# Kernel tuning notes

Measured on AMD Instinct MI355X. Metric: run time of the kernel, lower is better.

The kernel has to match this reference:

```python
import jax, jax.numpy as jnp
import numpy as np

N, E, IN, OUT = 50000, 800000, 128, 128
R = 5  # num_rels + 1 (last slice is the self-loop weight)


def setup_inputs() -> dict:
    key = jax.random.key(0)
    k = jax.random.split(key, 6)
    x = jax.random.normal(k[0], (N, IN), jnp.float32)
    src = jax.random.randint(k[1], (E,), 0, N)
    dst = jax.random.randint(k[2], (E,), 0, N)
    rel = jax.random.randint(k[3], (E,), 0, R - 1)  # edge rel_type in [0, num_rels)
    xavier = np.sqrt(2.0) * np.sqrt(6.0 / (IN + OUT))  # gain('relu') * xavier bound scale
    weight = jax.random.uniform(k[4], (R, IN, OUT), jnp.float32, -xavier, xavier)
    bias = jax.random.uniform(k[5], (R, OUT), jnp.float32, -xavier, xavier)
    return dict(x=x, weight=weight, bias=bias, src=src, dst=dst, rel=rel)


def reference(x, weight, bias, src, dst, rel):
    num_nodes = x.shape[0]
    num_edge_rels = weight.shape[0] - 1
    x_src = x[src]  # [E, IN] per-edge source gather
    # Per-edge message: x_src @ weight[rel] + bias[rel].
    # Grouped-GEMM style: one dense GEMM per relation, select by mask
    # (avoids materializing [E, IN, OUT] per-edge weights).
    msg = jnp.zeros((src.shape[0], weight.shape[2]), x.dtype)
    for r in range(num_edge_rels):
        hr = x_src @ weight[r] + bias[r]  # [E, OUT]
        msg = jnp.where((rel == r)[:, None], hr, msg)
    # Max-aggregation onto destination nodes; DGL fills 0 for nodes w/o in-edges.
    agg = jax.ops.segment_max(msg, dst, num_segments=num_nodes)  # [N, OUT]
    deg = jax.ops.segment_sum(jnp.ones_like(dst, jnp.float32), dst, num_segments=num_nodes)
    agg = jnp.where((deg > 0)[:, None], agg, jnp.zeros((), x.dtype))
    # Self-loop transform with last weight/bias slice.
    h = x @ weight[-1] + bias[-1] + agg
    return h
```

## Files before the change

### kernel.cpp

```cpp
#include <hip/hip_runtime.h>

#define NNODES 50000
#define NEDGES 800000
#define DIM    128
#define NRELS  4
#define NBLK2  25
#define DBLK   128
#define NDB    (5*DBLK)
#define NFB    3125
#define EPB    12500
#define NHC    64
#define RNG    25000
#define NPB    782

typedef __attribute__((ext_vector_type(8))) short bf16x8;
typedef __attribute__((ext_vector_type(8))) unsigned short u16x8;
typedef __attribute__((ext_vector_type(4))) float f32x4;

#define SSRC_OFF 0
#define CNT_OFF  3200000
#define BSUM_OFF 3404800
#define RANK_OFF 3405056
#define PCNT_OFF 5005056
#define WT_OFF   11405056
#define XBF_OFF  11568896
#define H_OFF    24368896

__device__ __forceinline__ unsigned short f2bf(float f) {
  unsigned u = __float_as_uint(f);
  return (unsigned short)((u + 0x7FFFu + ((u >> 16) & 1u)) >> 16);
}

__global__ __launch_bounds__(1024) void k_ph(
    const float* __restrict__ x, unsigned short* __restrict__ xbf,
    const float* __restrict__ W, unsigned short* __restrict__ Wt,
    const int* __restrict__ dst, unsigned short* __restrict__ rank,
    unsigned short* __restrict__ pcnt) {
  __shared__ unsigned lh[RNG / 2];
  if (blockIdx.x < NHC * 2) {
    int c = blockIdx.x >> 1;
    int r0 = (blockIdx.x & 1) * RNG;
    for (int i = threadIdx.x; i < RNG / 2; i += 1024) lh[i] = 0u;
    __syncthreads();
    int e0 = c * EPB;
    for (int e = e0 + threadIdx.x; e < e0 + EPB; e += 1024) {
      int d = dst[e] - r0;
      if ((unsigned)d < (unsigned)RNG) {
        unsigned old = atomicAdd(&lh[d >> 1], (d & 1) ? 65536u : 1u);
        rank[e] = (unsigned short)((old >> ((d & 1) << 4)) & 0xFFFFu);
      }
    }
    __syncthreads();
    unsigned* prow = (unsigned*)(pcnt + (size_t)c * NNODES + r0);
    for (int i = threadIdx.x; i < RNG / 2; i += 1024) prow[i] = lh[i];
    return;
  }
  int i = (blockIdx.x - NHC * 2) * 1024 + threadIdx.x;
  if (i < NNODES * DIM / 8) {
    const float4* p = (const float4*)x + i * 2;
    float4 v0 = p[0], v1 = p[1];
    u16x8 o;
    o[0] = f2bf(v0.x); o[1] = f2bf(v0.y); o[2] = f2bf(v0.z); o[3] = f2bf(v0.w);
    o[4] = f2bf(v1.x); o[5] = f2bf(v1.y); o[6] = f2bf(v1.z); o[7] = f2bf(v1.w);
    *(u16x8*)(xbf + i * 8) = o;
  }
  if (i < 5 * DIM * DIM) {
    int r = i >> 14, rem = i & 16383, k = rem >> 7, c = rem & 127;
    Wt[(r << 14) + (c << 7) + k] = f2bf(W[i]);
  }
}

__global__ void k_scanB(unsigned short* __restrict__ pcnt, unsigned* __restrict__ cnt,
                        unsigned* __restrict__ bsum) {
  __shared__ unsigned sh[256];
  int tid = threadIdx.x;
  int bin0 = blockIdx.x * 2048 + tid * 8;
  unsigned run[8] = {0, 0, 0, 0, 0, 0, 0, 0};
  if (bin0 < NNODES) {
    for (int b = 0; b < NHC; b++) {
      size_t off = (size_t)b * NNODES + bin0;
      u16x8 v = *(const u16x8*)(pcnt + off);
      u16x8 w;
#pragma unroll
      for (int j = 0; j < 8; j++) { w[j] = (unsigned short)run[j]; run[j] += v[j]; }
      *(u16x8*)(pcnt + off) = w;
    }
  }
  unsigned tsum = 0;
#pragma unroll
  for (int j = 0; j < 8; j++) tsum += run[j];
  sh[tid] = tsum;
  __syncthreads();
  for (int off = 1; off < 256; off <<= 1) {
    unsigned t = (tid >= off) ? sh[tid - off] : 0u;
    __syncthreads();
    sh[tid] += t;
    __syncthreads();
  }
  unsigned r = sh[tid] - tsum;
#pragma unroll
  for (int j = 0; j < 8; j++) { unsigned t = run[j]; cnt[bin0 + j] = r; r += t; }
  if (tid == 255) bsum[blockIdx.x] = sh[255];
}

__global__ void k_fix(unsigned* __restrict__ cnt, const unsigned* __restrict__ bsum) {
  int blk = blockIdx.x;
  if (blk == 0) return;
  unsigned p = 0;
  for (int k = 0; k < blk; k++) p += bsum[k];
  int base = blk * 2048 + threadIdx.x * 8;
#pragma unroll
  for (int j = 0; j < 8; j++) cnt[base + j] += p;
}

__global__ __launch_bounds__(256, 2) void k_dfill(
    const unsigned short* __restrict__ xbf, const unsigned short* __restrict__ Wt,
    const float* __restrict__ bias, unsigned short* __restrict__ H,
    float* __restrict__ out, const int* __restrict__ rel, const int* __restrict__ dst,
    const int* __restrict__ src, const unsigned* __restrict__ cnt,
    const unsigned short* __restrict__ rank, const unsigned short* __restrict__ pfx,
    unsigned* __restrict__ ssrc) {
  if (blockIdx.x >= NDB) {
    int e = (blockIdx.x - NDB) * 256 + threadIdx.x;
    if (e < NEDGES) {
      int r = rel[e]; r = r < 0 ? 0 : (r > NRELS - 1 ? NRELS - 1 : r);
      int d = dst[e];
      unsigned pos = cnt[d] + (unsigned)pfx[(size_t)(e / EPB) * NNODES + d] + (unsigned)rank[e];
      ssrc[pos] = (unsigned)(r * NNODES + src[e]);
    }
    return;
  }
  __shared__ unsigned short st[4][2048];
  int lane = threadIdx.x & 63;
  int wv = threadIdx.x >> 6;
  int r = blockIdx.x / DBLK;
  const int NT = NNODES / 16;
  int col = lane & 15, quad = lane >> 4;

  const unsigned short* wr = Wt + (r << 14);
  bf16x8 B[8][4];
  float bs[8];
#pragma unroll
  for (int ct = 0; ct < 8; ct++) {
#pragma unroll
    for (int kk = 0; kk < 4; kk++)
      B[ct][kk] = *(const bf16x8*)(wr + ((ct * 16 + col) << 7) + kk * 32 + quad * 8);
    bs[ct] = bias[(r << 7) + ct * 16 + col];
  }

  for (int t = (blockIdx.x % DBLK) * 4 + wv; t < NT; t += DBLK * 4) {
    int n0 = t * 16;
    int na = n0 + col;
    bf16x8 a0 = *(const bf16x8*)(xbf + (na << 7) + quad * 8);
    bf16x8 a1 = *(const bf16x8*)(xbf + (na << 7) + 32 + quad * 8);
    bf16x8 a2 = *(const bf16x8*)(xbf + (na << 7) + 64 + quad * 8);
    bf16x8 a3 = *(const bf16x8*)(xbf + (na << 7) + 96 + quad * 8);

    if (r < NRELS) {
#pragma unroll
      for (int ct = 0; ct < 8; ct++) {
        f32x4 acc = {0.f, 0.f, 0.f, 0.f};
        acc = __builtin_amdgcn_mfma_f32_16x16x32_bf16(a0, B[ct][0], acc, 0, 0, 0);
        acc = __builtin_amdgcn_mfma_f32_16x16x32_bf16(a1, B[ct][1], acc, 0, 0, 0);
        acc = __builtin_amdgcn_mfma_f32_16x16x32_bf16(a2, B[ct][2], acc, 0, 0, 0);
        acc = __builtin_amdgcn_mfma_f32_16x16x32_bf16(a3, B[ct][3], acc, 0, 0, 0);
        int cc = ct * 16 + col;
#pragma unroll
        for (int j = 0; j < 4; j++) st[wv][(quad * 4 + j) * 128 + cc] = f2bf(acc[j] + bs[ct]);
      }
      unsigned short* gb = H + (((size_t)(r * NNODES + n0)) << 7);
#pragma unroll
      for (int s = 0; s < 4; s++) {
        int off = s * 512 + lane * 8;
        __builtin_nontemporal_store(*(const u16x8*)(&st[wv][off]), (u16x8*)(gb + off));
      }
    } else {
#pragma unroll
      for (int ct = 0; ct < 8; ct++) {
        f32x4 acc = {0.f, 0.f, 0.f, 0.f};
        acc = __builtin_amdgcn_mfma_f32_16x16x32_bf16(a0, B[ct][0], acc, 0, 0, 0);
        acc = __builtin_amdgcn_mfma_f32_16x16x32_bf16(a1, B[ct][1], acc, 0, 0, 0);
        acc = __builtin_amdgcn_mfma_f32_16x16x32_bf16(a2, B[ct][2], acc, 0, 0, 0);
        acc = __builtin_amdgcn_mfma_f32_16x16x32_bf16(a3, B[ct][3], acc, 0, 0, 0);
        int cc = ct * 16 + col;
#pragma unroll
        for (int j = 0; j < 4; j++)
          __builtin_nontemporal_store(acc[j] + bs[ct],
                                      out + ((size_t)(n0 + quad * 4 + j) << 7) + (unsigned)cc);
      }
    }
  }
}

__global__ __launch_bounds__(256, 4) void k_agg(
    const unsigned* __restrict__ cnt, const unsigned* __restrict__ ssrc,
    const uint4* __restrict__ H4, float* __restrict__ out) {
  int lane = threadIdx.x & 15;
  int q = threadIdx.x >> 4;
  int n = blockIdx.x * 16 + q;
  unsigned base = cnt[n];
  int deg = (int)(cnt[n + 1] - base);

  float m0 = -3.0e38f, m1 = -3.0e38f, m2 = -3.0e38f, m3 = -3.0e38f;
  float m4 = -3.0e38f, m5 = -3.0e38f, m6 = -3.0e38f, m7 = -3.0e38f;
#define UNP(v)                                          \
  m0 = fmaxf(m0, __uint_as_float((v).x << 16));         \
  m1 = fmaxf(m1, __uint_as_float((v).x & 0xFFFF0000u)); \
  m2 = fmaxf(m2, __uint_as_float((v).y << 16));         \
  m3 = fmaxf(m3, __uint_as_float((v).y & 0xFFFF0000u)); \
  m4 = fmaxf(m4, __uint_as_float((v).z << 16));         \
  m5 = fmaxf(m5, __uint_as_float((v).z & 0xFFFF0000u)); \
  m6 = fmaxf(m6, __uint_as_float((v).w << 16));         \
  m7 = fmaxf(m7, __uint_as_float((v).w & 0xFFFF0000u))
  if (deg > 0) {
    int lim = deg - 1;
    for (int i = 0; i < deg; i += 8) {
      unsigned c0 = ssrc[base + min(i, lim)];
      unsigned c1 = ssrc[base + min(i + 1, lim)];
      unsigned c2 = ssrc[base + min(i + 2, lim)];
      unsigned c3 = ssrc[base + min(i + 3, lim)];
      unsigned c4 = ssrc[base + min(i + 4, lim)];
      unsigned c5 = ssrc[base + min(i + 5, lim)];
      unsigned c6 = ssrc[base + min(i + 6, lim)];
      unsigned c7 = ssrc[base + min(i + 7, lim)];
      uint4 v0 = H4[((size_t)c0 << 4) + lane];
      uint4 v1 = H4[((size_t)c1 << 4) + lane];
      uint4 v2 = H4[((size_t)c2 << 4) + lane];
      uint4 v3 = H4[((size_t)c3 << 4) + lane];
      uint4 v4 = H4[((size_t)c4 << 4) + lane];
      uint4 v5 = H4[((size_t)c5 << 4) + lane];
      uint4 v6 = H4[((size_t)c6 << 4) + lane];
      uint4 v7 = H4[((size_t)c7 << 4) + lane];
      UNP(v0); UNP(v1); UNP(v2); UNP(v3);
      UNP(v4); UNP(v5); UNP(v6); UNP(v7);
    }
  }
#undef UNP
  float4* op = (float4*)(out + ((size_t)n << 7)) + lane * 2;
  float4 s0 = op[0], s1 = op[1];
  if (deg > 0) {
    s0.x += m0; s0.y += m1; s0.z += m2; s0.w += m3;
    s1.x += m4; s1.y += m5; s1.z += m6; s1.w += m7;
  }
  op[0] = s0; op[1] = s1;
}

extern "C" void kernel_launch(void* const* d_in, const int* in_sizes, int n_in,
                              void* d_out, int out_size, void* d_ws, size_t ws_size,
                              hipStream_t stream) {
  const float* x = (const float*)d_in[0];
  const float* W = (const float*)d_in[1];
  const float* bias = (const float*)d_in[2];
  const int* src = (const int*)d_in[3];
  const int* dst = (const int*)d_in[4];
  const int* rel = (const int*)d_in[5];

  char* ws = (char*)d_ws;
  unsigned* ssrc = (unsigned*)(ws + SSRC_OFF);
  unsigned* cnt = (unsigned*)(ws + CNT_OFF);
  unsigned* bsum = (unsigned*)(ws + BSUM_OFF);
  unsigned short* rank = (unsigned short*)(ws + RANK_OFF);
  unsigned short* pcnt = (unsigned short*)(ws + PCNT_OFF);
  unsigned short* Wt = (unsigned short*)(ws + WT_OFF);
  unsigned short* xbf = (unsigned short*)(ws + XBF_OFF);
  unsigned short* H = (unsigned short*)(ws + H_OFF);
  float* out = (float*)d_out;

  hipLaunchKernelGGL(k_ph, dim3(NHC * 2 + NPB), dim3(1024), 0, stream, x, xbf, W, Wt, dst, rank,
                     pcnt);
  hipLaunchKernelGGL(k_scanB, dim3(NBLK2), dim3(256), 0, stream, pcnt, cnt, bsum);
  hipLaunchKernelGGL(k_fix, dim3(NBLK2), dim3(256), 0, stream, cnt, bsum);
  hipLaunchKernelGGL(k_dfill, dim3(NDB + NFB), dim3(256), 0, stream, xbf, Wt, bias, H, out, rel,
                     dst, src, cnt, rank, pcnt, ssrc);
  hipLaunchKernelGGL(k_agg, dim3(3125), dim3(256), 0, stream, cnt, ssrc, (const uint4*)H, out);
}
```

Baseline: 180.1 us.

## Fuse self-loop GEMM into aggregation kernel and split column scan

The self-loop transform (x @ W[4] + bias[4]) moves out of the dense-fill kernel and into the aggregation kernel. Each block computes its 16 nodes' self-loop rows with MFMA and adds the per-node max staged in shared memory, so the fp32 output is written once instead of written then read-modified-written. The per-column prefix over histogram chunks also moves into its own kernel with one thread per node, followed by a separate block scan. This costs an extra launch, a shared-memory sync and W reloads per aggregation block.

```diff
diff --git a/kernel.cpp b/kernel.cpp
--- a/kernel.cpp
+++ b/kernel.cpp
@@ -6,7 +6,7 @@
 #define NRELS  4
 #define NBLK2  25
 #define DBLK   128
-#define NDB    (5*DBLK)
+#define NDB    (4*DBLK)
 #define NFB    3125
 #define EPB    12500
 #define NHC    64
@@ -70,25 +70,30 @@
   }
 }
 
-__global__ void k_scanB(unsigned short* __restrict__ pcnt, unsigned* __restrict__ cnt,
-                        unsigned* __restrict__ bsum) {
+__global__ void k_scanC(unsigned short* __restrict__ pcnt, unsigned* __restrict__ cnt) {
+  int d = blockIdx.x * 256 + threadIdx.x;
+  if (d < NNODES) {
+    unsigned run = 0;
+#pragma unroll 8
+    for (int b = 0; b < NHC; b++) {
+      size_t off = (size_t)b * NNODES + d;
+      unsigned v = pcnt[off];
+      pcnt[off] = (unsigned short)run;
+      run += v;
+    }
+    cnt[d] = run;
+  } else {
+    cnt[d] = 0;
+  }
+}
+
+__global__ void k_scanA(unsigned* __restrict__ cnt, unsigned* __restrict__ bsum) {
   __shared__ unsigned sh[256];
   int tid = threadIdx.x;
-  int bin0 = blockIdx.x * 2048 + tid * 8;
-  unsigned run[8] = {0, 0, 0, 0, 0, 0, 0, 0};
-  if (bin0 < NNODES) {
-    for (int b = 0; b < NHC; b++) {
-      size_t off = (size_t)b * NNODES + bin0;
-      u16x8 v = *(const u16x8*)(pcnt + off);
-      u16x8 w;
-#pragma unroll
-      for (int j = 0; j < 8; j++) { w[j] = (unsigned short)run[j]; run[j] += v[j]; }
-      *(u16x8*)(pcnt + off) = w;
-    }
-  }
-  unsigned tsum = 0;
-#pragma unroll
-  for (int j = 0; j < 8; j++) tsum += run[j];
+  int base = blockIdx.x * 2048 + tid * 8;
+  unsigned v[8], tsum = 0;
+#pragma unroll
+  for (int j = 0; j < 8; j++) { v[j] = cnt[base + j]; tsum += v[j]; }
   sh[tid] = tsum;
   __syncthreads();
   for (int off = 1; off < 256; off <<= 1) {
@@ -97,9 +102,9 @@
     sh[tid] += t;
     __syncthreads();
   }
-  unsigned r = sh[tid] - tsum;
-#pragma unroll
-  for (int j = 0; j < 8; j++) { unsigned t = run[j]; cnt[bin0 + j] = r; r += t; }
+  unsigned run = sh[tid] - tsum;
+#pragma unroll
+  for (int j = 0; j < 8; j++) { unsigned t = v[j]; cnt[base + j] = run; run += t; }
   if (tid == 255) bsum[blockIdx.x] = sh[255];
 }
 
@@ -116,7 +121,7 @@
 __global__ __launch_bounds__(256, 2) void k_dfill(
     const unsigned short* __restrict__ xbf, const unsigned short* __restrict__ Wt,
     const float* __restrict__ bias, unsigned short* __restrict__ H,
-    float* __restrict__ out, const int* __restrict__ rel, const int* __restrict__ dst,
+    const int* __restrict__ rel, const int* __restrict__ dst,
     const int* __restrict__ src, const unsigned* __restrict__ cnt,
     const unsigned short* __restrict__ rank, const unsigned short* __restrict__ pfx,
     unsigned* __restrict__ ssrc) {
@@ -156,53 +161,43 @@
     bf16x8 a2 = *(const bf16x8*)(xbf + (na << 7) + 64 + quad * 8);
     bf16x8 a3 = *(const bf16x8*)(xbf + (na << 7) + 96 + quad * 8);
 
-    if (r < NRELS) {
-#pragma unroll
-      for (int ct = 0; ct < 8; ct++) {
-        f32x4 acc = {0.f, 0.f, 0.f, 0.f};
-        acc = __builtin_amdgcn_mfma_f32_16x16x32_bf16(a0, B[ct][0], acc, 0, 0, 0);
-        acc = __builtin_amdgcn_mfma_f32_16x16x32_bf16(a1, B[ct][1], acc, 0, 0, 0);
-        acc = __builtin_amdgcn_mfma_f32_16x16x32_bf16(a2, B[ct][2], acc, 0, 0, 0);
-        acc = __builtin_amdgcn_mfma_f32_16x16x32_bf16(a3, B[ct][3], acc, 0, 0, 0);
-        int cc = ct * 16 + col;
-#pragma unroll
-        for (int j = 0; j < 4; j++) st[wv][(quad * 4 + j) * 128 + cc] = f2bf(acc[j] + bs[ct]);
-      }
-      unsigned short* gb = H + (((size_t)(r * NNODES + n0)) << 7);
-#pragma unroll
-      for (int s = 0; s < 4; s++) {
-        int off = s * 512 + lane * 8;
-        __builtin_nontemporal_store(*(const u16x8*)(&st[wv][off]), (u16x8*)(gb + off));
-      }
-    } else {
-#pragma unroll
-      for (int ct = 0; ct < 8; ct++) {
-        f32x4 acc = {0.f, 0.f, 0.f, 0.f};
-        acc = __builtin_amdgcn_mfma_f32_16x16x32_bf16(a0, B[ct][0], acc, 0, 0, 0);
-        acc = __builtin_amdgcn_mfma_f32_16x16x32_bf16(a1, B[ct][1], acc, 0, 0, 0);
-        acc = __builtin_amdgcn_mfma_f32_16x16x32_bf16(a2, B[ct][2], acc, 0, 0, 0);
-        acc = __builtin_amdgcn_mfma_f32_16x16x32_bf16(a3, B[ct][3], acc, 0, 0, 0);
-        int cc = ct * 16 + col;
-#pragma unroll
-        for (int j = 0; j < 4; j++)
-          __builtin_nontemporal_store(acc[j] + bs[ct],
-                                      out + ((size_t)(n0 + quad * 4 + j) << 7) + (unsigned)cc);
-      }
+#pragma unroll
+    for (int ct = 0; ct < 8; ct++) {
+      f32x4 acc = {0.f, 0.f, 0.f, 0.f};
+      acc = __builtin_amdgcn_mfma_f32_16x16x32_bf16(a0, B[ct][0], acc, 0, 0, 0);
+      acc = __builtin_amdgcn_mfma_f32_16x16x32_bf16(a1, B[ct][1], acc, 0, 0, 0);
+      acc = __builtin_amdgcn_mfma_f32_16x16x32_bf16(a2, B[ct][2], acc, 0, 0, 0);
+      acc = __builtin_amdgcn_mfma_f32_16x16x32_bf16(a3, B[ct][3], acc, 0, 0, 0);
+      int cc = ct * 16 + col;
+#pragma unroll
+      for (int j = 0; j < 4; j++) st[wv][(quad * 4 + j) * 128 + cc] = f2bf(acc[j] + bs[ct]);
+    }
+    unsigned short* gb = H + (((size_t)(r * NNODES + n0)) << 7);
+#pragma unroll
+    for (int s = 0; s < 4; s++) {
+      int off = s * 512 + lane * 8;
+      __builtin_nontemporal_store(*(const u16x8*)(&st[wv][off]), (u16x8*)(gb + off));
     }
   }
 }
 
 __global__ __launch_bounds__(256, 4) void k_agg(
     const unsigned* __restrict__ cnt, const unsigned* __restrict__ ssrc,
-    const uint4* __restrict__ H4, float* __restrict__ out) {
-  int lane = threadIdx.x & 15;
-  int q = threadIdx.x >> 4;
-  int n = blockIdx.x * 16 + q;
+    const uint4* __restrict__ H4, const unsigned short* __restrict__ xbf,
+    const unsigned short* __restrict__ Wt, const float* __restrict__ bias,
+    float* __restrict__ out) {
+  __shared__ float smax[16][128];
+  int tid = threadIdx.x;
+  int n0 = blockIdx.x * 16;
+
+  int lane16 = tid & 15;
+  int q = tid >> 4;
+  int n = n0 + q;
   unsigned base = cnt[n];
   int deg = (int)(cnt[n + 1] - base);
-
-  float m0 = -3.0e38f, m1 = -3.0e38f, m2 = -3.0e38f, m3 = -3.0e38f;
-  float m4 = -3.0e38f, m5 = -3.0e38f, m6 = -3.0e38f, m7 = -3.0e38f;
+  float init = (deg > 0) ? -3.0e38f : 0.0f;
+  float m0 = init, m1 = init, m2 = init, m3 = init;
+  float m4 = init, m5 = init, m6 = init, m7 = init;
 #define UNP(v)                                          \
   m0 = fmaxf(m0, __uint_as_float((v).x << 16));         \
   m1 = fmaxf(m1, __uint_as_float((v).x & 0xFFFF0000u)); \
@@ -223,26 +218,54 @@
       unsigned c5 = ssrc[base + min(i + 5, lim)];
       unsigned c6 = ssrc[base + min(i + 6, lim)];
       unsigned c7 = ssrc[base + min(i + 7, lim)];
-      uint4 v0 = H4[((size_t)c0 << 4) + lane];
-      uint4 v1 = H4[((size_t)c1 << 4) + lane];
-      uint4 v2 = H4[((size_t)c2 << 4) + lane];
-      uint4 v3 = H4[((size_t)c3 << 4) + lane];
-      uint4 v4 = H4[((size_t)c4 << 4) + lane];
-      uint4 v5 = H4[((size_t)c5 << 4) + lane];
-      uint4 v6 = H4[((size_t)c6 << 4) + lane];
-      uint4 v7 = H4[((size_t)c7 << 4) + lane];
+      uint4 v0 = H4[((size_t)c0 << 4) + lane16];
+      uint4 v1 = H4[((size_t)c1 << 4) + lane16];
+      uint4 v2 = H4[((size_t)c2 << 4) + lane16];
+      uint4 v3 = H4[((size_t)c3 << 4) + lane16];
+      uint4 v4 = H4[((size_t)c4 << 4) + lane16];
+      uint4 v5 = H4[((size_t)c5 << 4) + lane16];
+      uint4 v6 = H4[((size_t)c6 << 4) + lane16];
+      uint4 v7 = H4[((size_t)c7 << 4) + lane16];
       UNP(v0); UNP(v1); UNP(v2); UNP(v3);
       UNP(v4); UNP(v5); UNP(v6); UNP(v7);
     }
   }
 #undef UNP
-  float4* op = (float4*)(out + ((size_t)n << 7)) + lane * 2;
-  float4 s0 = op[0], s1 = op[1];
-  if (deg > 0) {
-    s0.x += m0; s0.y += m1; s0.z += m2; s0.w += m3;
-    s1.x += m4; s1.y += m5; s1.z += m6; s1.w += m7;
-  }
-  op[0] = s0; op[1] = s1;
+  float4* sp = (float4*)&smax[q][lane16 * 8];
+  sp[0] = (float4){m0, m1, m2, m3};
+  sp[1] = (float4){m4, m5, m6, m7};
+  __syncthreads();
+
+  int l64 = tid & 63;
+  int wv = tid >> 6;
+  int col = l64 & 15, quad = l64 >> 4;
+  const unsigned short* wr = Wt + (4 << 14);
+  int na = n0 + col;
+  bf16x8 a0 = *(const bf16x8*)(xbf + (na << 7) + quad * 8);
+  bf16x8 a1 = *(const bf16x8*)(xbf + (na << 7) + 32 + quad * 8);
+  bf16x8 a2 = *(const bf16x8*)(xbf + (na << 7) + 64 + quad * 8);
+  bf16x8 a3 = *(const bf16x8*)(xbf + (na << 7) + 96 + quad * 8);
+#pragma unroll
+  for (int cti = 0; cti < 2; cti++) {
+    int ct = wv * 2 + cti;
+    bf16x8 b0 = *(const bf16x8*)(wr + ((ct * 16 + col) << 7) + 0 * 32 + quad * 8);
+    bf16x8 b1 = *(const bf16x8*)(wr + ((ct * 16 + col) << 7) + 1 * 32 + quad * 8);
+    bf16x8 b2 = *(const bf16x8*)(wr + ((ct * 16 + col) << 7) + 2 * 32 + quad * 8);
+    bf16x8 b3 = *(const bf16x8*)(wr + ((ct * 16 + col) << 7) + 3 * 32 + quad * 8);
+    float bsv = bias[(4 << 7) + ct * 16 + col];
+    f32x4 acc = {0.f, 0.f, 0.f, 0.f};
+    acc = __builtin_amdgcn_mfma_f32_16x16x32_bf16(a0, b0, acc, 0, 0, 0);
+    acc = __builtin_amdgcn_mfma_f32_16x16x32_bf16(a1, b1, acc, 0, 0, 0);
+    acc = __builtin_amdgcn_mfma_f32_16x16x32_bf16(a2, b2, acc, 0, 0, 0);
+    acc = __builtin_amdgcn_mfma_f32_16x16x32_bf16(a3, b3, acc, 0, 0, 0);
+    int cc = ct * 16 + col;
+#pragma unroll
+    for (int j = 0; j < 4; j++) {
+      int row = quad * 4 + j;
+      __builtin_nontemporal_store(acc[j] + bsv + smax[row][cc],
+                                  out + ((size_t)(n0 + row) << 7) + (unsigned)cc);
+    }
+  }
 }
 
 extern "C" void kernel_launch(void* const* d_in, const int* in_sizes, int n_in,
@@ -268,9 +291,11 @@
 
   hipLaunchKernelGGL(k_ph, dim3(NHC * 2 + NPB), dim3(1024), 0, stream, x, xbf, W, Wt, dst, rank,
                      pcnt);
-  hipLaunchKernelGGL(k_scanB, dim3(NBLK2), dim3(256), 0, stream, pcnt, cnt, bsum);
+  hipLaunchKernelGGL(k_scanC, dim3(200), dim3(256), 0, stream, pcnt, cnt);
+  hipLaunchKernelGGL(k_scanA, dim3(NBLK2), dim3(256), 0, stream, cnt, bsum);
   hipLaunchKernelGGL(k_fix, dim3(NBLK2), dim3(256), 0, stream, cnt, bsum);
-  hipLaunchKernelGGL(k_dfill, dim3(NDB + NFB), dim3(256), 0, stream, xbf, Wt, bias, H, out, rel,
+  hipLaunchKernelGGL(k_dfill, dim3(NDB + NFB), dim3(256), 0, stream, xbf, Wt, bias, H, rel,
                      dst, src, cnt, rank, pcnt, ssrc);
-  hipLaunchKernelGGL(k_agg, dim3(3125), dim3(256), 0, stream, cnt, ssrc, (const uint4*)H, out);
-}
+  hipLaunchKernelGGL(k_agg, dim3(3125), dim3(256), 0, stream, cnt, ssrc, (const uint4*)H, xbf,
+                     Wt, bias, out);
+}
```

New measurement: 184.6 us. +2.5%, slower.

## Merge scan and fixup kernels into one grid-synchronized scan over more blocks

Applied to the files above, without the earlier changes.

Replaces the two-kernel scan (25 blocks, 8 bins per thread) plus a fixup kernel with a single scan kernel of 200 blocks, one bin per thread. Blocks publish their totals to a global array and spin on an atomic counter until all blocks have arrived, then each sums the preceding block totals itself. This removes one kernel launch and spreads the column walk across more CUs. It relies on all 200 blocks being co-resident so the spin-wait cannot deadlock, and reading 16-bit elements one at a time loses the previous vectorized loads.

```diff
diff --git a/kernel.cpp b/kernel.cpp
--- a/kernel.cpp
+++ b/kernel.cpp
@@ -4,7 +4,6 @@
 #define NEDGES 800000
 #define DIM    128
 #define NRELS  4
-#define NBLK2  25
 #define DBLK   128
 #define NDB    (5*DBLK)
 #define NFB    3125
@@ -12,6 +11,7 @@
 #define NHC    64
 #define RNG    25000
 #define NPB    782
+#define SCB    200
 
 typedef __attribute__((ext_vector_type(8))) short bf16x8;
 typedef __attribute__((ext_vector_type(8))) unsigned short u16x8;
@@ -20,11 +20,11 @@
 #define SSRC_OFF 0
 #define CNT_OFF  3200000
 #define BSUM_OFF 3404800
-#define RANK_OFF 3405056
-#define PCNT_OFF 5005056
-#define WT_OFF   11405056
-#define XBF_OFF  11568896
-#define H_OFF    24368896
+#define RANK_OFF 3405824
+#define PCNT_OFF 5005824
+#define WT_OFF   11405824
+#define XBF_OFF  11569664
+#define H_OFF    24369664
 
 __device__ __forceinline__ unsigned short f2bf(float f) {
   unsigned u = __float_as_uint(f);
@@ -35,9 +35,10 @@
     const float* __restrict__ x, unsigned short* __restrict__ xbf,
     const float* __restrict__ W, unsigned short* __restrict__ Wt,
     const int* __restrict__ dst, unsigned short* __restrict__ rank,
-    unsigned short* __restrict__ pcnt) {
+    unsigned short* __restrict__ pcnt, unsigned* flag) {
   __shared__ unsigned lh[RNG / 2];
   if (blockIdx.x < NHC * 2) {
+    if (blockIdx.x == 0 && threadIdx.x == 0) atomicExch(flag, 0u);
     int c = blockIdx.x >> 1;
     int r0 = (blockIdx.x & 1) * RNG;
     for (int i = threadIdx.x; i < RNG / 2; i += 1024) lh[i] = 0u;
@@ -70,26 +71,23 @@
   }
 }
 
-__global__ void k_scanB(unsigned short* __restrict__ pcnt, unsigned* __restrict__ cnt,
-                        unsigned* __restrict__ bsum) {
+__global__ __launch_bounds__(256) void k_scan(unsigned short* __restrict__ pcnt,
+                                              unsigned* __restrict__ cnt,
+                                              unsigned* bsum, unsigned* flag) {
   __shared__ unsigned sh[256];
-  int tid = threadIdx.x;
-  int bin0 = blockIdx.x * 2048 + tid * 8;
-  unsigned run[8] = {0, 0, 0, 0, 0, 0, 0, 0};
-  if (bin0 < NNODES) {
+  int tid = threadIdx.x, blk = blockIdx.x;
+  int d = blk * 256 + tid;
+  unsigned run = 0;
+  if (d < NNODES) {
+#pragma unroll 8
     for (int b = 0; b < NHC; b++) {
-      size_t off = (size_t)b * NNODES + bin0;
-      u16x8 v = *(const u16x8*)(pcnt + off);
-      u16x8 w;
-#pragma unroll
-      for (int j = 0; j < 8; j++) { w[j] = (unsigned short)run[j]; run[j] += v[j]; }
-      *(u16x8*)(pcnt + off) = w;
-    }
-  }
-  unsigned tsum = 0;
-#pragma unroll
-  for (int j = 0; j < 8; j++) tsum += run[j];
-  sh[tid] = tsum;
+      size_t off = (size_t)b * NNODES + d;
+      unsigned v = pcnt[off];
+      pcnt[off] = (unsigned short)run;
+      run += v;
+    }
+  }
+  sh[tid] = run;
   __syncthreads();
   for (int off = 1; off < 256; off <<= 1) {
     unsigned t = (tid >= off) ? sh[tid - off] : 0u;
@@ -97,20 +95,23 @@
     sh[tid] += t;
     __syncthreads();
   }
-  unsigned r = sh[tid] - tsum;
-#pragma unroll
-  for (int j = 0; j < 8; j++) { unsigned t = run[j]; cnt[bin0 + j] = r; r += t; }
-  if (tid == 255) bsum[blockIdx.x] = sh[255];
-}
-
-__global__ void k_fix(unsigned* __restrict__ cnt, const unsigned* __restrict__ bsum) {
-  int blk = blockIdx.x;
-  if (blk == 0) return;
-  unsigned p = 0;
-  for (int k = 0; k < blk; k++) p += bsum[k];
-  int base = blk * 2048 + threadIdx.x * 8;
-#pragma unroll
-  for (int j = 0; j < 8; j++) cnt[base + j] += p;
+  unsigned excl = sh[tid] - run;
+  unsigned btot = sh[255];
+  __syncthreads();
+  if (tid == 0) {
+    atomicExch(&bsum[blk], btot);
+    atomicAdd(flag, 1u);
+    while (atomicAdd(flag, 0u) < SCB) { __builtin_amdgcn_s_sleep(8); }
+  }
+  __syncthreads();
+  unsigned pv = (tid < blk) ? atomicAdd(&bsum[tid], 0u) : 0u;
+  sh[tid] = pv;
+  __syncthreads();
+  for (int off = 128; off > 0; off >>= 1) {
+    if (tid < off) sh[tid] += sh[tid + off];
+    __syncthreads();
+  }
+  cnt[d] = sh[0] + excl;
 }
 
 __global__ __launch_bounds__(256, 2) void k_dfill(
@@ -259,6 +260,7 @@
   unsigned* ssrc = (unsigned*)(ws + SSRC_OFF);
   unsigned* cnt = (unsigned*)(ws + CNT_OFF);
   unsigned* bsum = (unsigned*)(ws + BSUM_OFF);
+  unsigned* flag = (unsigned*)(ws + BSUM_OFF + 800);
   unsigned short* rank = (unsigned short*)(ws + RANK_OFF);
   unsigned short* pcnt = (unsigned short*)(ws + PCNT_OFF);
   unsigned short* Wt = (unsigned short*)(ws + WT_OFF);
@@ -267,9 +269,8 @@
   float* out = (float*)d_out;
 
   hipLaunchKernelGGL(k_ph, dim3(NHC * 2 + NPB), dim3(1024), 0, stream, x, xbf, W, Wt, dst, rank,
-                     pcnt);
-  hipLaunchKernelGGL(k_scanB, dim3(NBLK2), dim3(256), 0, stream, pcnt, cnt, bsum);
-  hipLaunchKernelGGL(k_fix, dim3(NBLK2), dim3(256), 0, stream, cnt, bsum);
+                     pcnt, flag);
+  hipLaunchKernelGGL(k_scan, dim3(SCB), dim3(256), 0, stream, pcnt, cnt, bsum, flag);
   hipLaunchKernelGGL(k_dfill, dim3(NDB + NFB), dim3(256), 0, stream, xbf, Wt, bias, H, out, rel,
                      dst, src, cnt, rank, pcnt, ssrc);
   hipLaunchKernelGGL(k_agg, dim3(3125), dim3(256), 0, stream, cnt, ssrc, (const uint4*)H, out);
```

After: 180.8 us. About the same (+0.4%).
